# Kernel optimization log

Measured on AMD Instinct MI355X. Metric: run time of the kernel, lower is better.

The kernel has to match this reference:

```python
import jax, jax.numpy as jnp
import numpy as np

B, DZ, DS, DH = 8192, 1024, 64, 4096

def setup_inputs() -> dict:
    key = jax.random.key(0)
    ks = jax.random.split(key, 8)
    r1 = 1.0 / np.sqrt(DZ)   # W1 init range (last dim dz)
    r2 = 1.0 / np.sqrt(DH)   # W2 init range (last dim dim_hidden)
    rc = 1.0 / np.sqrt(DS)   # C init range
    return {
        "z": jax.random.normal(ks[0], (B, DZ), jnp.float32),
        "s": jax.random.normal(ks[1], (B, DS), jnp.float32),
        "A": jnp.full((DZ,), 0.95, jnp.float32),
        "W1": jax.random.uniform(ks[2], (DH, DZ), jnp.float32, -r1, r1),
        "W2": jax.random.uniform(ks[3], (DZ, DH), jnp.float32, -r2, r2),
        "h1": jax.random.normal(ks[4], (DH,), jnp.float32),
        "h2": jax.random.normal(ks[5], (DZ,), jnp.float32),
        "C": jax.random.uniform(ks[6], (DZ, DS), jnp.float32, -rc, rc),
    }

def reference(z, s, A, W1, W2, h1, h2, C):
    # PLRNN step, W_trial=False, mean_center=False, noise=0:
    # z' = A*z + relu(z @ W1.T + h1) @ W2.T + h2 + s @ C.T
    z_activated = jax.nn.relu(z @ W1.T + h1)          # [B, DH]
    return A * z + z_activated @ W2.T + h2 + s @ C.T  # [B, DZ]
```

## Files before the change

### kernel.cpp

```cpp
#include <hip/hip_runtime.h>

#define BB 8192
#define DZ 1024
#define DS 64
#define DH 4096
#define KEXT (DH + DS)

typedef float floatx4 __attribute__((ext_vector_type(4)));
typedef __bf16 bf16x8 __attribute__((ext_vector_type(8)));
typedef __attribute__((address_space(1))) void* as1_void_ptr;
typedef __attribute__((address_space(3))) void* as3_void_ptr;

__device__ __forceinline__ void async_copy16(const void* g, void* l) {
    __builtin_amdgcn_global_load_lds((as1_void_ptr)g, (as3_void_ptr)l, 16, 0, 0);
}

__global__ void prep_all(const float* __restrict__ z, const float* __restrict__ W1,
                         const float* __restrict__ W2, const float* __restrict__ C,
                         const float* __restrict__ s,
                         __bf16* __restrict__ zb, __bf16* __restrict__ W1b,
                         __bf16* __restrict__ B2b, __bf16* __restrict__ Hb) {
    const int b = blockIdx.x, t = threadIdx.x;
    if (b < 8192) {
        int i = b * 256 + t;
        float4 v = ((const float4*)z)[i];
        __bf16* o = zb + (size_t)i * 4;
        o[0] = (__bf16)v.x; o[1] = (__bf16)v.y; o[2] = (__bf16)v.z; o[3] = (__bf16)v.w;
    } else if (b < 12288) {
        int i = (b - 8192) * 256 + t;
        float4 v = ((const float4*)W1)[i];
        __bf16* o = W1b + (size_t)i * 4;
        o[0] = (__bf16)v.x; o[1] = (__bf16)v.y; o[2] = (__bf16)v.z; o[3] = (__bf16)v.w;
    } else if (b < 13312) {
        int j = b - 12288;
        for (int h = t; h < KEXT; h += 256) {
            float v = (h < DH) ? W2[(size_t)j * DH + h] : C[(size_t)j * DS + (h - DH)];
            B2b[(size_t)j * KEXT + h] = (__bf16)v;
        }
    } else {
        int i = (b - 13312) * 256 + t;
        int r = i >> 6, k = i & 63;
        Hb[(size_t)r * KEXT + DH + k] = (__bf16)s[i];
    }
}


__global__ __launch_bounds__(256) void gemm1_relu(
    const __bf16* __restrict__ Ag, const __bf16* __restrict__ Bg,
    const float* __restrict__ h1, __bf16* __restrict__ Hb)
{
    constexpr int ldA = DZ, ldB = DZ, KITER = DZ / 64;
    __shared__ __align__(16) __bf16 As[2 * 128 * 32];
    __shared__ __align__(16) __bf16 Bs[2 * 128 * 32];

    const int tid = threadIdx.x;
    const int wave = tid >> 6, lane = tid & 63;
    const int wm = wave >> 1, wn = wave & 1;
    const int row0 = blockIdx.x * 128;
    const int col0 = blockIdx.y * 128;

    const __bf16* pA = Ag + (size_t)(row0 + (tid >> 2)) * ldA + (tid & 3) * 8;
    const __bf16* pB = Bg + (size_t)(col0 + (tid >> 2)) * ldB + (tid & 3) * 8;
    __bf16* dA0 = As + wave * 16 * 32;
    __bf16* dB0 = Bs + wave * 16 * 32;

    const __bf16* Afrag = As + (wm * 64 + (lane & 15)) * 32 + (lane >> 4) * 8;
    const __bf16* Bfrag = Bs + (wn * 64 + (lane & 15)) * 32 + (lane >> 4) * 8;

    floatx4 acc[4][4];
#pragma unroll
    for (int i = 0; i < 4; ++i)
#pragma unroll
        for (int j = 0; j < 4; ++j) acc[i][j] = (floatx4)0.0f;

    for (int kt = 0; kt < KITER; ++kt) {
        const __bf16* ak = pA + kt * 64;
        const __bf16* bk = pB + kt * 64;
        async_copy16(ak,                         dA0);
        async_copy16(ak + (size_t)64 * ldA,      dA0 + 64 * 32);
        async_copy16(ak + 32,                    dA0 + 128 * 32);
        async_copy16(ak + (size_t)64 * ldA + 32, dA0 + 128 * 32 + 64 * 32);
        async_copy16(bk,                         dB0);
        async_copy16(bk + (size_t)64 * ldB,      dB0 + 64 * 32);
        async_copy16(bk + 32,                    dB0 + 128 * 32);
        async_copy16(bk + (size_t)64 * ldB + 32, dB0 + 128 * 32 + 64 * 32);
        __builtin_amdgcn_s_waitcnt(0);
        __syncthreads();

#pragma unroll
        for (int ks = 0; ks < 2; ++ks) {
            bf16x8 af[4], bfr[4];
#pragma unroll
            for (int i = 0; i < 4; ++i) af[i] = *(const bf16x8*)(Afrag + ks * 4096 + i * 16 * 32);
#pragma unroll
            for (int j = 0; j < 4; ++j) bfr[j] = *(const bf16x8*)(Bfrag + ks * 4096 + j * 16 * 32);
#pragma unroll
            for (int i = 0; i < 4; ++i)
#pragma unroll
                for (int j = 0; j < 4; ++j)
                    acc[i][j] = __builtin_amdgcn_mfma_f32_16x16x32_bf16(af[i], bfr[j], acc[i][j], 0, 0, 0);
        }
        __syncthreads();
    }

    const int r0 = row0 + wm * 64 + (lane >> 4) * 4;
    const int c0 = col0 + wn * 64 + (lane & 15);
#pragma unroll
    for (int i = 0; i < 4; ++i) {
#pragma unroll
        for (int j = 0; j < 4; ++j) {
            int c = c0 + j * 16;
            float bias = h1[c];
#pragma unroll
            for (int rg = 0; rg < 4; ++rg) {
                int r = r0 + i * 16 + rg;
                float v = acc[i][j][rg] + bias;
                v = v > 0.0f ? v : 0.0f;
                Hb[(size_t)r * KEXT + c] = (__bf16)v;
            }
        }
    }
}

__global__ __launch_bounds__(256) void gemm2_out(
    const __bf16* __restrict__ Ag, const __bf16* __restrict__ Bg,
    const float* __restrict__ Adiag, const float* __restrict__ h2,
    const __bf16* __restrict__ zb, float* __restrict__ out)
{
    constexpr int ldA = KEXT, ldB = KEXT, KITER = KEXT / 64;
    __shared__ __align__(16) __bf16 As[2 * 128 * 32];
    __shared__ __align__(16) __bf16 Bs[2 * 128 * 32];

    const int tid = threadIdx.x;
    const int wave = tid >> 6, lane = tid & 63;
    const int wm = wave >> 1, wn = wave & 1;
    const int row0 = blockIdx.x * 128;
    const int col0 = blockIdx.y * 128;

    const __bf16* pA = Ag + (size_t)(row0 + (tid >> 2)) * ldA + (tid & 3) * 8;
    const __bf16* pB = Bg + (size_t)(col0 + (tid >> 2)) * ldB + (tid & 3) * 8;
    __bf16* dA0 = As + wave * 16 * 32;
    __bf16* dB0 = Bs + wave * 16 * 32;

    const __bf16* Afrag = As + (wm * 64 + (lane & 15)) * 32 + (lane >> 4) * 8;
    const __bf16* Bfrag = Bs + (wn * 64 + (lane & 15)) * 32 + (lane >> 4) * 8;

    floatx4 acc[4][4];
#pragma unroll
    for (int i = 0; i < 4; ++i)
#pragma unroll
        for (int j = 0; j < 4; ++j) acc[i][j] = (floatx4)0.0f;

    for (int kt = 0; kt < KITER; ++kt) {
        const __bf16* ak = pA + kt * 64;
        const __bf16* bk = pB + kt * 64;
        async_copy16(ak,                         dA0);
        async_copy16(ak + (size_t)64 * ldA,      dA0 + 64 * 32);
        async_copy16(ak + 32,                    dA0 + 128 * 32);
        async_copy16(ak + (size_t)64 * ldA + 32, dA0 + 128 * 32 + 64 * 32);
        async_copy16(bk,                         dB0);
        async_copy16(bk + (size_t)64 * ldB,      dB0 + 64 * 32);
        async_copy16(bk + 32,                    dB0 + 128 * 32);
        async_copy16(bk + (size_t)64 * ldB + 32, dB0 + 128 * 32 + 64 * 32);
        __builtin_amdgcn_s_waitcnt(0);
        __syncthreads();

#pragma unroll
        for (int ks = 0; ks < 2; ++ks) {
            bf16x8 af[4], bfr[4];
#pragma unroll
            for (int i = 0; i < 4; ++i) af[i] = *(const bf16x8*)(Afrag + ks * 4096 + i * 16 * 32);
#pragma unroll
            for (int j = 0; j < 4; ++j) bfr[j] = *(const bf16x8*)(Bfrag + ks * 4096 + j * 16 * 32);
#pragma unroll
            for (int i = 0; i < 4; ++i)
#pragma unroll
                for (int j = 0; j < 4; ++j)
                    acc[i][j] = __builtin_amdgcn_mfma_f32_16x16x32_bf16(af[i], bfr[j], acc[i][j], 0, 0, 0);
        }
        __syncthreads();
    }

    const int r0 = row0 + wm * 64 + (lane >> 4) * 4;
    const int c0 = col0 + wn * 64 + (lane & 15);
#pragma unroll
    for (int i = 0; i < 4; ++i) {
#pragma unroll
        for (int j = 0; j < 4; ++j) {
            const int c = c0 + j * 16;
            const float aj = Adiag[c];
            const float hj = h2[c];
#pragma unroll
            for (int rg = 0; rg < 4; ++rg) {
                const int r = r0 + i * 16 + rg;
                out[(size_t)r * DZ + c] =
                    acc[i][j][rg] + aj * (float)zb[(size_t)r * DZ + c] + hj;
            }
        }
    }
}


extern "C" void kernel_launch(void* const* d_in, const int* in_sizes, int n_in,
                              void* d_out, int out_size, void* d_ws, size_t ws_size,
                              hipStream_t stream) {
    const float* z  = (const float*)d_in[0];
    const float* s  = (const float*)d_in[1];
    const float* A  = (const float*)d_in[2];
    const float* W1 = (const float*)d_in[3];
    const float* W2 = (const float*)d_in[4];
    const float* h1 = (const float*)d_in[5];
    const float* h2 = (const float*)d_in[6];
    const float* C  = (const float*)d_in[7];
    float* out = (float*)d_out;

    char* ws = (char*)d_ws;
    size_t offHb  = 0;
    size_t offZb  = offHb  + (size_t)BB * KEXT * 2;
    size_t offW1b = offZb  + (size_t)BB * DZ * 2;
    size_t offB2b = offW1b + (size_t)DH * DZ * 2;
    __bf16* Hb  = (__bf16*)(ws + offHb);
    __bf16* zb  = (__bf16*)(ws + offZb);
    __bf16* W1b = (__bf16*)(ws + offW1b);
    __bf16* B2b = (__bf16*)(ws + offB2b);

    prep_all<<<15360, 256, 0, stream>>>(z, W1, W2, C, s, zb, W1b, B2b, Hb);
    gemm1_relu<<<dim3(BB / 128, DH / 128), 256, 0, stream>>>(zb, W1b, h1, Hb);
    gemm2_out<<<dim3(BB / 128, DZ / 128), 256, 0, stream>>>(Hb, B2b, A, h2, zb, out);
}
```

Before: 282.2 us.

## Enlarge GEMM tiles to 256x128 with 512 threads, double-buffer gemm2, vectorize prep

Both GEMMs move to 512-thread blocks covering 256 rows by 128 columns, so each B tile loaded into LDS is shared by twice as many rows and global traffic per flop drops. gemm2 adds a two-stage LDS double buffer with explicit vmcnt waits and raw barriers, so the next K-slice loads while the current one runs on MFMA. The prep kernel now converts to bf16 with vector stores and handles the s columns with float4 loads, which cuts the number of memory instructions. In exchange, LDS use and register pressure per block go up and there are fewer blocks in each grid, which can lower occupancy.

New measurement: 259.6 us. -8.0%, faster.

```diff
diff --git a/kernel.cpp b/kernel.cpp
--- a/kernel.cpp
+++ b/kernel.cpp
@@ -8,11 +8,21 @@
 
 typedef float floatx4 __attribute__((ext_vector_type(4)));
 typedef __bf16 bf16x8 __attribute__((ext_vector_type(8)));
+typedef __bf16 bf16x4 __attribute__((ext_vector_type(4)));
 typedef __attribute__((address_space(1))) void* as1_void_ptr;
 typedef __attribute__((address_space(3))) void* as3_void_ptr;
 
+#define WAIT_VM0   3952
+#define WAIT_VM6   3958
+#define WAIT_LGKM0 49279
+
 __device__ __forceinline__ void async_copy16(const void* g, void* l) {
     __builtin_amdgcn_global_load_lds((as1_void_ptr)g, (as3_void_ptr)l, 16, 0, 0);
+}
+
+__device__ __forceinline__ bf16x4 cvt4(float4 v) {
+    bf16x4 o = { (__bf16)v.x, (__bf16)v.y, (__bf16)v.z, (__bf16)v.w };
+    return o;
 }
 
 __global__ void prep_all(const float* __restrict__ z, const float* __restrict__ W1,
@@ -23,46 +33,48 @@
     const int b = blockIdx.x, t = threadIdx.x;
     if (b < 8192) {
         int i = b * 256 + t;
-        float4 v = ((const float4*)z)[i];
-        __bf16* o = zb + (size_t)i * 4;
-        o[0] = (__bf16)v.x; o[1] = (__bf16)v.y; o[2] = (__bf16)v.z; o[3] = (__bf16)v.w;
+        *(bf16x4*)(zb + (size_t)i * 4) = cvt4(((const float4*)z)[i]);
     } else if (b < 12288) {
         int i = (b - 8192) * 256 + t;
-        float4 v = ((const float4*)W1)[i];
-        __bf16* o = W1b + (size_t)i * 4;
-        o[0] = (__bf16)v.x; o[1] = (__bf16)v.y; o[2] = (__bf16)v.z; o[3] = (__bf16)v.w;
+        *(bf16x4*)(W1b + (size_t)i * 4) = cvt4(((const float4*)W1)[i]);
     } else if (b < 13312) {
         int j = b - 12288;
-        for (int h = t; h < KEXT; h += 256) {
-            float v = (h < DH) ? W2[(size_t)j * DH + h] : C[(size_t)j * DS + (h - DH)];
-            B2b[(size_t)j * KEXT + h] = (__bf16)v;
+        const float* wrow = W2 + (size_t)j * DH;
+        const float* crow = C + (size_t)j * DS;
+        __bf16* orow = B2b + (size_t)j * KEXT;
+        for (int c = t; c < 520; c += 256) {
+            int h = c * 8;
+            const float* src = (h < DH) ? (wrow + h) : (crow + (h - DH));
+            *(bf16x4*)(orow + h)     = cvt4(*(const float4*)(src));
+            *(bf16x4*)(orow + h + 4) = cvt4(*(const float4*)(src + 4));
         }
     } else {
         int i = (b - 13312) * 256 + t;
-        int r = i >> 6, k = i & 63;
-        Hb[(size_t)r * KEXT + DH + k] = (__bf16)s[i];
-    }
-}
-
-
-__global__ __launch_bounds__(256) void gemm1_relu(
+        int r = i >> 4, k = (i & 15) * 4;
+        float4 v = *(const float4*)(s + (size_t)r * DS + k);
+        *(bf16x4*)(Hb + (size_t)r * KEXT + DH + k) = cvt4(v);
+    }
+}
+
+
+__global__ __launch_bounds__(512, 4) void gemm1_relu(
     const __bf16* __restrict__ Ag, const __bf16* __restrict__ Bg,
     const float* __restrict__ h1, __bf16* __restrict__ Hb)
 {
     constexpr int ldA = DZ, ldB = DZ, KITER = DZ / 64;
-    __shared__ __align__(16) __bf16 As[2 * 128 * 32];
-    __shared__ __align__(16) __bf16 Bs[2 * 128 * 32];
+    __shared__ __align__(16) __bf16 As[256 * 64];
+    __shared__ __align__(16) __bf16 Bs[128 * 64];
 
     const int tid = threadIdx.x;
     const int wave = tid >> 6, lane = tid & 63;
     const int wm = wave >> 1, wn = wave & 1;
-    const int row0 = blockIdx.x * 128;
+    const int row0 = blockIdx.x * 256;
     const int col0 = blockIdx.y * 128;
 
     const __bf16* pA = Ag + (size_t)(row0 + (tid >> 2)) * ldA + (tid & 3) * 8;
-    const __bf16* pB = Bg + (size_t)(col0 + (tid >> 2)) * ldB + (tid & 3) * 8;
-    __bf16* dA0 = As + wave * 16 * 32;
-    __bf16* dB0 = Bs + wave * 16 * 32;
+    const __bf16* pB = Bg + (size_t)(col0 + ((tid >> 2) & 127)) * ldB + (tid & 3) * 8;
+    __bf16* lA = As + wave * 512;
+    __bf16* lB = Bs + wave * 512;
 
     const __bf16* Afrag = As + (wm * 64 + (lane & 15)) * 32 + (lane >> 4) * 8;
     const __bf16* Bfrag = Bs + (wn * 64 + (lane & 15)) * 32 + (lane >> 4) * 8;
@@ -76,14 +88,12 @@
     for (int kt = 0; kt < KITER; ++kt) {
         const __bf16* ak = pA + kt * 64;
         const __bf16* bk = pB + kt * 64;
-        async_copy16(ak,                         dA0);
-        async_copy16(ak + (size_t)64 * ldA,      dA0 + 64 * 32);
-        async_copy16(ak + 32,                    dA0 + 128 * 32);
-        async_copy16(ak + (size_t)64 * ldA + 32, dA0 + 128 * 32 + 64 * 32);
-        async_copy16(bk,                         dB0);
-        async_copy16(bk + (size_t)64 * ldB,      dB0 + 64 * 32);
-        async_copy16(bk + 32,                    dB0 + 128 * 32);
-        async_copy16(bk + (size_t)64 * ldB + 32, dB0 + 128 * 32 + 64 * 32);
+        async_copy16(ak,                           lA);
+        async_copy16(ak + (size_t)128 * ldA,       lA + 4096);
+        async_copy16(ak + 32,                      lA + 8192);
+        async_copy16(ak + (size_t)128 * ldA + 32,  lA + 8192 + 4096);
+        async_copy16(bk,                           lB);
+        async_copy16(bk + 32,                      lB + 4096);
         __builtin_amdgcn_s_waitcnt(0);
         __syncthreads();
 
@@ -91,7 +101,7 @@
         for (int ks = 0; ks < 2; ++ks) {
             bf16x8 af[4], bfr[4];
 #pragma unroll
-            for (int i = 0; i < 4; ++i) af[i] = *(const bf16x8*)(Afrag + ks * 4096 + i * 16 * 32);
+            for (int i = 0; i < 4; ++i) af[i] = *(const bf16x8*)(Afrag + ks * 8192 + i * 16 * 32);
 #pragma unroll
             for (int j = 0; j < 4; ++j) bfr[j] = *(const bf16x8*)(Bfrag + ks * 4096 + j * 16 * 32);
 #pragma unroll
@@ -122,25 +132,23 @@
     }
 }
 
-__global__ __launch_bounds__(256) void gemm2_out(
+__global__ __launch_bounds__(512, 2) void gemm2_out(
     const __bf16* __restrict__ Ag, const __bf16* __restrict__ Bg,
     const float* __restrict__ Adiag, const float* __restrict__ h2,
     const __bf16* __restrict__ zb, float* __restrict__ out)
 {
     constexpr int ldA = KEXT, ldB = KEXT, KITER = KEXT / 64;
-    __shared__ __align__(16) __bf16 As[2 * 128 * 32];
-    __shared__ __align__(16) __bf16 Bs[2 * 128 * 32];
+    __shared__ __align__(16) __bf16 As[2 * 256 * 64];
+    __shared__ __align__(16) __bf16 Bs[2 * 128 * 64];
 
     const int tid = threadIdx.x;
     const int wave = tid >> 6, lane = tid & 63;
     const int wm = wave >> 1, wn = wave & 1;
-    const int row0 = blockIdx.x * 128;
+    const int row0 = blockIdx.x * 256;
     const int col0 = blockIdx.y * 128;
 
     const __bf16* pA = Ag + (size_t)(row0 + (tid >> 2)) * ldA + (tid & 3) * 8;
-    const __bf16* pB = Bg + (size_t)(col0 + (tid >> 2)) * ldB + (tid & 3) * 8;
-    __bf16* dA0 = As + wave * 16 * 32;
-    __bf16* dB0 = Bs + wave * 16 * 32;
+    const __bf16* pB = Bg + (size_t)(col0 + ((tid >> 2) & 127)) * ldB + (tid & 3) * 8;
 
     const __bf16* Afrag = As + (wm * 64 + (lane & 15)) * 32 + (lane >> 4) * 8;
     const __bf16* Bfrag = Bs + (wn * 64 + (lane & 15)) * 32 + (lane >> 4) * 8;
@@ -151,34 +159,49 @@
 #pragma unroll
         for (int j = 0; j < 4; ++j) acc[i][j] = (floatx4)0.0f;
 
-    for (int kt = 0; kt < KITER; ++kt) {
+    auto issue = [&](int kt, int q) {
         const __bf16* ak = pA + kt * 64;
         const __bf16* bk = pB + kt * 64;
-        async_copy16(ak,                         dA0);
-        async_copy16(ak + (size_t)64 * ldA,      dA0 + 64 * 32);
-        async_copy16(ak + 32,                    dA0 + 128 * 32);
-        async_copy16(ak + (size_t)64 * ldA + 32, dA0 + 128 * 32 + 64 * 32);
-        async_copy16(bk,                         dB0);
-        async_copy16(bk + (size_t)64 * ldB,      dB0 + 64 * 32);
-        async_copy16(bk + 32,                    dB0 + 128 * 32);
-        async_copy16(bk + (size_t)64 * ldB + 32, dB0 + 128 * 32 + 64 * 32);
-        __builtin_amdgcn_s_waitcnt(0);
-        __syncthreads();
+        __bf16* lA = As + q * 16384 + wave * 512;
+        __bf16* lB = Bs + q * 8192  + wave * 512;
+        async_copy16(ak,                           lA);
+        async_copy16(ak + (size_t)128 * ldA,       lA + 4096);
+        async_copy16(ak + 32,                      lA + 8192);
+        async_copy16(ak + (size_t)128 * ldA + 32,  lA + 8192 + 4096);
+        async_copy16(bk,                           lB);
+        async_copy16(bk + 32,                      lB + 4096);
+    };
+
+    issue(0, 0);
+
+    for (int kt = 0; kt < KITER; ++kt) {
+        const int p = kt & 1;
+        if (kt + 1 < KITER) {
+            issue(kt + 1, p ^ 1);
+            __builtin_amdgcn_s_waitcnt(WAIT_VM6);
+        } else {
+            __builtin_amdgcn_s_waitcnt(WAIT_VM0);
+        }
+        __builtin_amdgcn_s_barrier();
 
 #pragma unroll
         for (int ks = 0; ks < 2; ++ks) {
+            const __bf16* Ab = Afrag + p * 16384 + ks * 8192;
+            const __bf16* Bb = Bfrag + p * 8192  + ks * 4096;
             bf16x8 af[4], bfr[4];
 #pragma unroll
-            for (int i = 0; i < 4; ++i) af[i] = *(const bf16x8*)(Afrag + ks * 4096 + i * 16 * 32);
-#pragma unroll
-            for (int j = 0; j < 4; ++j) bfr[j] = *(const bf16x8*)(Bfrag + ks * 4096 + j * 16 * 32);
+            for (int i = 0; i < 4; ++i) af[i] = *(const bf16x8*)(Ab + i * 16 * 32);
+#pragma unroll
+            for (int j = 0; j < 4; ++j) bfr[j] = *(const bf16x8*)(Bb + j * 16 * 32);
 #pragma unroll
             for (int i = 0; i < 4; ++i)
 #pragma unroll
                 for (int j = 0; j < 4; ++j)
                     acc[i][j] = __builtin_amdgcn_mfma_f32_16x16x32_bf16(af[i], bfr[j], acc[i][j], 0, 0, 0);
         }
-        __syncthreads();
+
+        __builtin_amdgcn_s_waitcnt(WAIT_LGKM0);
+        __builtin_amdgcn_s_barrier();
     }
 
     const int r0 = row0 + wm * 64 + (lane >> 4) * 4;
@@ -224,7 +247,7 @@
     __bf16* W1b = (__bf16*)(ws + offW1b);
     __bf16* B2b = (__bf16*)(ws + offB2b);
 
-    prep_all<<<15360, 256, 0, stream>>>(z, W1, W2, C, s, zb, W1b, B2b, Hb);
-    gemm1_relu<<<dim3(BB / 128, DH / 128), 256, 0, stream>>>(zb, W1b, h1, Hb);
-    gemm2_out<<<dim3(BB / 128, DZ / 128), 256, 0, stream>>>(Hb, B2b, A, h2, zb, out);
-}
+    prep_all<<<13824, 256, 0, stream>>>(z, W1, W2, C, s, zb, W1b, B2b, Hb);
+    gemm1_relu<<<dim3(BB / 256, DH / 128), 512, 0, stream>>>(zb, W1b, h1, Hb);
+    gemm2_out<<<dim3(BB / 256, DZ / 128), 512, 0, stream>>>(Hb, B2b, A, h2, zb, out);
+}
```
